# Performance work log

Measured on AMD Instinct MI355X. Metric: run time of the kernel, lower is better.

The kernel has to match this reference:

```python
import jax, jax.numpy as jnp
import numpy as np
import math

B, D, H, N, L = 32, 64, 8, 4096, 12
DK = D // H  # 8
APT = 10

def conv1x1_relu(x, w, b):
    # x: [B, C, N, L]; w: [O, C]; b: [O]  (1x1 conv == channel matmul)
    return jax.nn.relu(jnp.einsum('oc,bcnl->bonl', w, x) + b[None, :, None, None])

def setup_inputs() -> dict:
    key = jax.random.key(0)
    ks = jax.random.split(key, 12)
    s = 1.0 / math.sqrt(D)
    return {
        'x': jax.random.normal(ks[0], (B, D, N, L), jnp.float32),
        'wq': jax.random.normal(ks[1], (D, D), jnp.float32) * s,
        'bq': jnp.zeros((D,), jnp.float32),
        'wv': jax.random.normal(ks[2], (D, D), jnp.float32) * s,
        'bv': jnp.zeros((D,), jnp.float32),
        'wc': jax.random.normal(ks[3], (D, D), jnp.float32) * s,
        'bc': jnp.zeros((D,), jnp.float32),
        'memory': jax.random.normal(ks[4], (H, L, N, DK), jnp.float32) * 0.02,
        'weight': jnp.ones((D, N, L), jnp.float32),
        'bias': jnp.zeros((D, N, L), jnp.float32),
        'nv1': jax.random.normal(ks[5], (N, APT), jnp.float32),
        'nv2': jax.random.normal(ks[6], (APT, N), jnp.float32),
    }

def reference(x, wq, bq, wv, bv, wc, bc, memory, weight, bias, nv1, nv2):
    scale = 1.0 / math.sqrt(DK)
    q = conv1x1_relu(x, wq, bq)               # [B, D, N, L]
    v = conv1x1_relu(x, wv, bv)               # [B, D, N, L]
    # [B, D, N, L] -> [B, H, dk, N, L] -> [B, H, L, N, dk]
    v5 = jnp.transpose(v.reshape(B, H, DK, N, L), (0, 1, 4, 3, 2))
    q5 = jnp.transpose(q.reshape(B, H, DK, N, L), (0, 1, 4, 3, 2))
    key_sm = jax.nn.softmax(memory * scale, axis=-1)       # [H, L, N, dk]
    q_sm = jax.nn.softmax(q5 * scale, axis=-1)             # [B, H, L, N, dk]
    Aapt = jax.nn.softmax(jax.nn.relu(nv1 @ nv2), axis=-1) # [N, N]
    kv = jnp.einsum('hlnx,bhlny->bhlxy', key_sm, v5)       # [B,H,L,dk,dk]
    attn_qkv = jnp.einsum('bhlnx,bhlxy->bhlny', q_sm, kv)  # [B,H,L,N,dk]
    # 'nm,bhlnc->bhlnc' sums Aapt over m -> row-sum scaling of value
    row = jnp.sum(Aapt, axis=1)                            # [N]
    attn_dyn = row[None, None, None, :, None] * v5
    y = attn_qkv + attn_dyn                                # [B,H,L,N,dk]
    y = jnp.transpose(y, (0, 1, 4, 3, 2)).reshape(B, D, N, L)
    y = conv1x1_relu(y, wc, bc)
    out = y * weight[None] + bias[None] + y
    return out
```

## Files before the change

### kernel.cpp

```cpp
#include <hip/hip_runtime.h>
#include <math.h>
#include <stdint.h>

#define BB 32
#define DD 64
#define HH 8
#define NNN 4096
#define LL 12
#define PP (NNN * LL)

#define NTILES_A 24
#define CHUNK_A (64 * NTILES_A)
#define NCHUNK_A (PP / CHUNK_A)

#define NTILES_B 12
#define CHUNK_B (64 * NTILES_B)
#define NCHUNK_B (PP / CHUNK_B)

#define VSTRIDE 68
#define SCALE 0.35355339059327373f

typedef const __attribute__((address_space(1))) uint32_t gu32;
typedef __attribute__((address_space(3))) uint32_t lu32;

__device__ __forceinline__ void dma16(const float* src, float* dst) {
    __builtin_amdgcn_global_load_lds((gu32*)src, (lu32*)dst, 16, 0, 0);
}

__global__ void prep(const float* __restrict__ wq, const float* __restrict__ wv,
                     const float* __restrict__ wc, float* __restrict__ wt)
{
    const int i = blockIdx.x * 256 + threadIdx.x;
    const int o = i >> 6, c = i & 63;
    wt[c * 64 + o]        = wq[i];
    wt[4096 + c * 64 + o] = wv[i];
    wt[8192 + c * 64 + o] = wc[i];
}

__global__ void prep_ksm(const float* __restrict__ mem, float* __restrict__ ksm)
{
    const int g = blockIdx.x * 256 + threadIdx.x;
    const int p = g >> 3, h = g & 7;
    const int n = p / 12, l = p - n * 12;
    const float4* mp = (const float4*)(mem + (((size_t)(h * 12 + l) * NNN + n) << 3));
    float4 a0 = mp[0], a1 = mp[1];
    float v0 = a0.x * SCALE, v1 = a0.y * SCALE, v2 = a0.z * SCALE, v3 = a0.w * SCALE;
    float v4 = a1.x * SCALE, v5 = a1.y * SCALE, v6 = a1.z * SCALE, v7 = a1.w * SCALE;
    float m = fmaxf(fmaxf(fmaxf(v0, v1), fmaxf(v2, v3)),
                    fmaxf(fmaxf(v4, v5), fmaxf(v6, v7)));
    float e0 = __expf(v0 - m), e1 = __expf(v1 - m), e2 = __expf(v2 - m), e3 = __expf(v3 - m);
    float e4 = __expf(v4 - m), e5 = __expf(v5 - m), e6 = __expf(v6 - m), e7 = __expf(v7 - m);
    float inv = 1.0f / (e0 + e1 + e2 + e3 + e4 + e5 + e6 + e7);
    float4* op = (float4*)(ksm + ((size_t)g << 3));
    op[0] = make_float4(e0 * inv, e1 * inv, e2 * inv, e3 * inv);
    op[1] = make_float4(e4 * inv, e5 * inv, e6 * inv, e7 * inv);
}

__global__ void prep_wb(const float* __restrict__ wgt, const float* __restrict__ bsa,
                        float* __restrict__ wb)
{
    const size_t i = (size_t)blockIdx.x * 256 + threadIdx.x;
    wb[i * 2]     = wgt[i] + 1.0f;
    wb[i * 2 + 1] = bsa[i];
}

__global__ __launch_bounds__(512, 2)
void pass_a(const float* __restrict__ x, const float* __restrict__ wvt,
            const float* __restrict__ bv, const float* __restrict__ mem,
            const float* __restrict__ ksm,
            float* __restrict__ kv)
{
    __shared__ float xb0[64 * 64];
    __shared__ float xb1[64 * 64];
    __shared__ float ksl[64 * 64];
    __shared__ float v_tile[64 * VSTRIDE];

    const int t = threadIdx.x;
    const int b = blockIdx.y;
    const int chunk0 = blockIdx.x * CHUNK_A;

    const int p1 = t & 63;
    const int og = t >> 6;
    const int o0 = og << 3;
    const int o0u = __builtin_amdgcn_readfirstlane(o0);
    const float* __restrict__ wvu = wvt + o0u;

    float bvl[8];
#pragma unroll
    for (int j = 0; j < 8; j++) bvl[j] = bv[o0 + j];

    const int wid = t >> 6;
    const int ln  = t & 63;
    const int g_r = ln >> 4;
    const int g_c4 = (ln & 15) << 2;

    const int h2 = (t >> 3) & 7;
    const int x2 = t & 7;
    const int l0 = t >> 6;
    const int l1 = 8 + (t >> 6);
    const bool has2 = (t < 256);

    float acc[2][8];
#pragma unroll
    for (int q = 0; q < 2; q++)
#pragma unroll
        for (int y = 0; y < 8; y++) acc[q][y] = 0.f;

    const float* xb = x + (size_t)(b * 64) * PP;

    auto issue_x = [&](float* dst, int pn) {
        const int r0 = wid << 3;
        dma16(xb + (size_t)(r0 + g_r) * PP + pn + g_c4, dst + (r0 << 6));
        dma16(xb + (size_t)(r0 + 4 + g_r) * PP + pn + g_c4, dst + ((r0 + 4) << 6));
    };
    auto issue_ks = [&](int pn) {
        const int fo = wid << 9;
        const float* s0 = ksm + (((size_t)pn) << 6) + fo + (ln << 2);
        dma16(s0, ksl + fo);
        dma16(s0 + 256, ksl + fo + 256);
    };
    auto fallback_ks = [&](int pbase) {
        int pos = t >> 3, h = t & 7;
        int pg = pbase + pos;
        int n = pg / 12;
        int l = pg - n * 12;
        const float4* mp = (const float4*)(mem + (((size_t)(h * 12 + l) * NNN + n) << 3));
        float4 a0 = mp[0], a1 = mp[1];
        float v0 = a0.x * SCALE, v1 = a0.y * SCALE, v2 = a0.z * SCALE, v3 = a0.w * SCALE;
        float v4 = a1.x * SCALE, v5 = a1.y * SCALE, v6 = a1.z * SCALE, v7 = a1.w * SCALE;
        float m = fmaxf(fmaxf(fmaxf(v0, v1), fmaxf(v2, v3)),
                        fmaxf(fmaxf(v4, v5), fmaxf(v6, v7)));
        float e0 = __expf(v0 - m), e1 = __expf(v1 - m), e2 = __expf(v2 - m), e3 = __expf(v3 - m);
        float e4 = __expf(v4 - m), e5 = __expf(v5 - m), e6 = __expf(v6 - m), e7 = __expf(v7 - m);
        float inv = 1.0f / (e0 + e1 + e2 + e3 + e4 + e5 + e6 + e7);
        float4* kp = (float4*)(ksl + (pos << 6) + (h << 3));
        kp[0] = make_float4(e0 * inv, e1 * inv, e2 * inv, e3 * inv);
        kp[1] = make_float4(e4 * inv, e5 * inv, e6 * inv, e7 * inv);
    };

    issue_x(xb0, chunk0);
    if (ksm) issue_ks(chunk0); else fallback_ks(chunk0);
    __syncthreads();

    for (int tile = 0; tile < NTILES_A; tile++) {
        const int pbase = chunk0 + tile * 64;
        float* bufA = (tile & 1) ? xb1 : xb0;
        float* bufB = (tile & 1) ? xb0 : xb1;
        const bool more = (tile + 1) < NTILES_A;

        if (more) issue_x(bufB, pbase + 64);

        float va[8];
#pragma unroll
        for (int j = 0; j < 8; j++) va[j] = 0.f;
        for (int c = 0; c < 64; c += 4) {
            float xs0 = bufA[(c << 6) + p1];
            float xs1 = bufA[((c + 1) << 6) + p1];
            float xs2 = bufA[((c + 2) << 6) + p1];
            float xs3 = bufA[((c + 3) << 6) + p1];
            const float* w0 = wvu + c * 64;
#pragma unroll
            for (int j = 0; j < 8; j++) {
                va[j] += w0[j] * xs0;
                va[j] += w0[64 + j] * xs1;
                va[j] += w0[128 + j] * xs2;
                va[j] += w0[192 + j] * xs3;
            }
        }
        {
            const int slot = ((og ^ (p1 >> 3)) & 7) << 3;
            float4* vt4 = (float4*)(v_tile + p1 * VSTRIDE + slot);
            float4 w;
            w.x = fmaxf(va[0] + bvl[0], 0.f);
            w.y = fmaxf(va[1] + bvl[1], 0.f);
            w.z = fmaxf(va[2] + bvl[2], 0.f);
            w.w = fmaxf(va[3] + bvl[3], 0.f);
            vt4[0] = w;
            w.x = fmaxf(va[4] + bvl[4], 0.f);
            w.y = fmaxf(va[5] + bvl[5], 0.f);
            w.z = fmaxf(va[6] + bvl[6], 0.f);
            w.w = fmaxf(va[7] + bvl[7], 0.f);
            vt4[1] = w;
        }
        __syncthreads();

        const int r = pbase % 12;
        {
            int s = l0 - r;
            if (s < 0) s += 12;
            for (int p = s; p < 64; p += 12) {
                float ksv = ksl[(p << 6) + (h2 << 3) + x2];
                const int slot = ((h2 ^ (p >> 3)) & 7) << 3;
                const float4* vp = (const float4*)(v_tile + p * VSTRIDE + slot);
                float4 u0 = vp[0], u1 = vp[1];
                acc[0][0] += ksv * u0.x; acc[0][1] += ksv * u0.y;
                acc[0][2] += ksv * u0.z; acc[0][3] += ksv * u0.w;
                acc[0][4] += ksv * u1.x; acc[0][5] += ksv * u1.y;
                acc[0][6] += ksv * u1.z; acc[0][7] += ksv * u1.w;
            }
        }
        if (has2) {
            int s = l1 - r;
            if (s < 0) s += 12;
            for (int p = s; p < 64; p += 12) {
                float ksv = ksl[(p << 6) + (h2 << 3) + x2];
                const int slot = ((h2 ^ (p >> 3)) & 7) << 3;
                const float4* vp = (const float4*)(v_tile + p * VSTRIDE + slot);
                float4 u0 = vp[0], u1 = vp[1];
                acc[1][0] += ksv * u0.x; acc[1][1] += ksv * u0.y;
                acc[1][2] += ksv * u0.z; acc[1][3] += ksv * u0.w;
                acc[1][4] += ksv * u1.x; acc[1][5] += ksv * u1.y;
                acc[1][6] += ksv * u1.z; acc[1][7] += ksv * u1.w;
            }
        }
        __syncthreads();

        if (more) { if (ksm) issue_ks(pbase + 64); else fallback_ks(pbase + 64); }
    }

    {
        float* kvp = kv + (((size_t)((b * 12 + l0) * 8 + h2)) << 6) + (x2 << 3);
#pragma unroll
        for (int y = 0; y < 8; y++) atomicAdd(kvp + y, acc[0][y]);
    }
    if (has2) {
        float* kvp = kv + (((size_t)((b * 12 + l1) * 8 + h2)) << 6) + (x2 << 3);
#pragma unroll
        for (int y = 0; y < 8; y++) atomicAdd(kvp + y, acc[1][y]);
    }
}

__global__ __launch_bounds__(256, 4)
void pass_b(const float* __restrict__ x, const float* __restrict__ wqt,
            const float* __restrict__ wvt, const float* __restrict__ wct,
            const float* __restrict__ bq, const float* __restrict__ bv,
            const float* __restrict__ bc, const float* __restrict__ kv,
            const float* __restrict__ wgt, const float* __restrict__ bsa,
            const float* __restrict__ wb,
            float* __restrict__ out)
{
    __shared__ float kv_lds[12 * 512];
    __shared__ float y_tile[64 * 64];

    const int t = threadIdx.x;
    const int b = blockIdx.y;
    const int chunk0 = blockIdx.x * CHUNK_B;

    const int p1 = t & 63;
    const int og = t >> 6;
    const int o0 = og << 4;
    const int o0u = __builtin_amdgcn_readfirstlane(o0);
    const float* __restrict__ wqu = wqt + o0u;
    const float* __restrict__ wvu = wvt + o0u;
    const float* __restrict__ wcu = wct + o0u;

    {
        const float* kvb = kv + (size_t)b * 6144;
        for (int i = t; i < 6144; i += 256) {
            const int l = i >> 9;
            const int h = (i >> 6) & 7;
            const int xx = (i >> 3) & 7;
            const int y = i & 7;
            kv_lds[(l << 9) + (h << 6) + ((xx ^ (l & 3)) << 3) + y] = kvb[i];
        }
    }

    float bql[16], bvl[16], bcl[16];
#pragma unroll
    for (int j = 0; j < 16; j++) {
        bql[j] = bq[o0 + j];
        bvl[j] = bv[o0 + j];
        bcl[j] = bc[o0 + j];
    }

    const float* xb = x + (size_t)(b * 64) * PP;
    float* ob = out + (size_t)(b * 64) * PP;

    __syncthreads();

    for (int tile_i = 0; tile_i < NTILES_B; tile_i++) {
        const int pbase = chunk0 + tile_i * 64;
        const int pg = pbase + p1;
        const int l = pg % 12;

        float qa[16], va[16];
#pragma unroll
        for (int j = 0; j < 16; j++) { qa[j] = 0.f; va[j] = 0.f; }
        const float* xp = xb + pg;
        for (int c = 0; c < 64; c += 4) {
            float xs0 = xp[(size_t)c * PP];
            float xs1 = xp[(size_t)(c + 1) * PP];
            float xs2 = xp[(size_t)(c + 2) * PP];
            float xs3 = xp[(size_t)(c + 3) * PP];
            const float* q0 = wqu + c * 64;
            const float* v0 = wvu + c * 64;
#pragma unroll
            for (int j = 0; j < 16; j++) {
                qa[j] += q0[j] * xs0;       va[j] += v0[j] * xs0;
                qa[j] += q0[64 + j] * xs1;  va[j] += v0[64 + j] * xs1;
                qa[j] += q0[128 + j] * xs2; va[j] += v0[128 + j] * xs2;
                qa[j] += q0[192 + j] * xs3; va[j] += v0[192 + j] * xs3;
            }
        }
#pragma unroll
        for (int j = 0; j < 16; j++) {
            qa[j] = fmaxf(qa[j] + bql[j], 0.f) * SCALE;
            va[j] = fmaxf(va[j] + bvl[j], 0.f);
        }

#pragma unroll
        for (int hh = 0; hh < 2; hh++) {
            float* qh = qa + hh * 8;
            float m = fmaxf(fmaxf(fmaxf(qh[0], qh[1]), fmaxf(qh[2], qh[3])),
                            fmaxf(fmaxf(qh[4], qh[5]), fmaxf(qh[6], qh[7])));
            float s = 0.f;
#pragma unroll
            for (int xk = 0; xk < 8; xk++) { qh[xk] = __expf(qh[xk] - m); s += qh[xk]; }
            float inv = 1.0f / s;
#pragma unroll
            for (int xk = 0; xk < 8; xk++) qh[xk] *= inv;
        }

        const int lsw = l & 3;
#pragma unroll
        for (int hh = 0; hh < 2; hh++) {
            const int h = og * 2 + hh;
            const float* kvp = kv_lds + (l << 9) + (h << 6);
            float yv[8];
#pragma unroll
            for (int y = 0; y < 8; y++) yv[y] = va[hh * 8 + y];
#pragma unroll
            for (int xk = 0; xk < 8; xk++) {
                float qv = qa[hh * 8 + xk];
                const float4* kp = (const float4*)(kvp + ((xk ^ lsw) << 3));
                float4 k0 = kp[0], k1 = kp[1];
                yv[0] += qv * k0.x; yv[1] += qv * k0.y;
                yv[2] += qv * k0.z; yv[3] += qv * k0.w;
                yv[4] += qv * k1.x; yv[5] += qv * k1.y;
                yv[6] += qv * k1.z; yv[7] += qv * k1.w;
            }
#pragma unroll
            for (int y = 0; y < 8; y++)
                y_tile[((o0 + hh * 8 + y) << 6) + p1] = yv[y];
        }
        __syncthreads();

        float ca[16];
#pragma unroll
        for (int j = 0; j < 16; j++) ca[j] = 0.f;
        for (int c = 0; c < 64; c += 4) {
            float y0 = y_tile[(c << 6) + p1];
            float y1 = y_tile[((c + 1) << 6) + p1];
            float y2 = y_tile[((c + 2) << 6) + p1];
            float y3 = y_tile[((c + 3) << 6) + p1];
            const float* w0 = wcu + c * 64;
#pragma unroll
            for (int j = 0; j < 16; j++) {
                ca[j] += w0[j] * y0;
                ca[j] += w0[64 + j] * y1;
                ca[j] += w0[128 + j] * y2;
                ca[j] += w0[192 + j] * y3;
            }
        }
        if (wb) {
#pragma unroll
            for (int j = 0; j < 16; j++) {
                float yc = fmaxf(ca[j] + bcl[j], 0.f);
                size_t oi = (size_t)(o0 + j) * PP + pg;
                float2 w2 = *(const float2*)(wb + oi * 2);
                ob[oi] = yc * w2.x + w2.y;
            }
        } else {
#pragma unroll
            for (int j = 0; j < 16; j++) {
                float yc = fmaxf(ca[j] + bcl[j], 0.f);
                size_t oi = (size_t)(o0 + j) * PP + pg;
                ob[oi] = yc * (wgt[oi] + 1.0f) + bsa[oi];
            }
        }
        __syncthreads();
    }
}

extern "C" void kernel_launch(void* const* d_in, const int* in_sizes, int n_in,
                              void* d_out, int out_size, void* d_ws, size_t ws_size,
                              hipStream_t stream) {
    const float* x   = (const float*)d_in[0];
    const float* wq  = (const float*)d_in[1];
    const float* bq  = (const float*)d_in[2];
    const float* wv  = (const float*)d_in[3];
    const float* bv  = (const float*)d_in[4];
    const float* wc  = (const float*)d_in[5];
    const float* bc  = (const float*)d_in[6];
    const float* mem = (const float*)d_in[7];
    const float* wgt = (const float*)d_in[8];
    const float* bsa = (const float*)d_in[9];
    float* outp = (float*)d_out;

    const size_t kv_floats  = (size_t)BB * LL * HH * 64;
    const size_t wt_floats  = 3 * 4096;
    const size_t ksm_floats = (size_t)PP * 64;
    const size_t wb_floats  = (size_t)PP * 64 * 2;

    float* kvw = (float*)d_ws;
    float* wt  = kvw + kv_floats;
    float* ksm = wt + wt_floats;
    float* wb  = ksm + ksm_floats;
    const bool have_ksm =
        ws_size >= (kv_floats + wt_floats + ksm_floats) * sizeof(float);
    const bool have_wb =
        ws_size >= (kv_floats + wt_floats + ksm_floats + wb_floats) * sizeof(float);

    hipMemsetAsync(kvw, 0, kv_floats * sizeof(float), stream);

    prep<<<16, 256, 0, stream>>>(wq, wv, wc, wt);
    if (have_ksm) {
        prep_ksm<<<(PP * 8) / 256, 256, 0, stream>>>(mem, ksm);
    }
    if (have_wb) {
        prep_wb<<<(PP * 64) / 256, 256, 0, stream>>>(wgt, bsa, wb);
    }

    dim3 grid_a(NCHUNK_A, BB);
    pass_a<<<grid_a, 512, 0, stream>>>(x, wt + 4096, bv, mem,
                                       have_ksm ? ksm : nullptr, kvw);
    dim3 grid_b(NCHUNK_B, BB);
    pass_b<<<grid_b, 256, 0, stream>>>(x, wt, wt + 4096, wt + 8192,
                                       bq, bv, bc, kvw, wgt, bsa,
                                       have_wb ? wb : nullptr, outp);
}
```

Baseline: 1.584 ms.

## Stage x tiles in swizzled LDS with register prefetch of next tile in pass_b

pass_b now loads each 64x64 x tile cooperatively with float4 global loads into a transposed, XOR-swizzled LDS buffer. The next tile is prefetched into registers while the output conv runs, then written to LDS before the barrier. The y tile uses the same swizzled layout, so both channel loops read a float4 per four channels instead of four scalar LDS or global loads. Launch bounds drop to 2 blocks per SM to make room for the extra registers and LDS, at the cost of lower occupancy.

```diff
diff --git a/kernel.cpp b/kernel.cpp
--- a/kernel.cpp
+++ b/kernel.cpp
@@ -25,6 +25,10 @@
 
 __device__ __forceinline__ void dma16(const float* src, float* dst) {
     __builtin_amdgcn_global_load_lds((gu32*)src, (lu32*)dst, 16, 0, 0);
+}
+
+__device__ __forceinline__ int xsw(int p, int c4) {
+    return (p << 6) + (((c4 ^ (p & 7)) & 15) << 2);
 }
 
 __global__ void prep(const float* __restrict__ wq, const float* __restrict__ wv,
@@ -230,7 +234,7 @@
     }
 }
 
-__global__ __launch_bounds__(256, 4)
+__global__ __launch_bounds__(256, 2)
 void pass_b(const float* __restrict__ x, const float* __restrict__ wqt,
             const float* __restrict__ wvt, const float* __restrict__ wct,
             const float* __restrict__ bq, const float* __restrict__ bv,
@@ -239,8 +243,9 @@
             const float* __restrict__ wb,
             float* __restrict__ out)
 {
+    __shared__ float xt[64 * 64];
+    __shared__ float yt[64 * 64];
     __shared__ float kv_lds[12 * 512];
-    __shared__ float y_tile[64 * 64];
 
     const int t = threadIdx.x;
     const int b = blockIdx.y;
@@ -253,6 +258,20 @@
     const float* __restrict__ wqu = wqt + o0u;
     const float* __restrict__ wvu = wvt + o0u;
     const float* __restrict__ wcu = wct + o0u;
+
+    const int sx_c  = t >> 4;
+    const int sx_p4 = (t & 15) << 2;
+
+    float bql[16], bvl[16], bcl[16];
+#pragma unroll
+    for (int j = 0; j < 16; j++) {
+        bql[j] = bq[o0 + j];
+        bvl[j] = bv[o0 + j];
+        bcl[j] = bc[o0 + j];
+    }
+
+    const float* xb = x + (size_t)(b * 64) * PP;
+    float* ob = out + (size_t)(b * 64) * PP;
 
     {
         const float* kvb = kv + (size_t)b * 6144;
@@ -263,43 +282,37 @@
             const int y = i & 7;
             kv_lds[(l << 9) + (h << 6) + ((xx ^ (l & 3)) << 3) + y] = kvb[i];
         }
-    }
-
-    float bql[16], bvl[16], bcl[16];
-#pragma unroll
-    for (int j = 0; j < 16; j++) {
-        bql[j] = bq[o0 + j];
-        bvl[j] = bv[o0 + j];
-        bcl[j] = bc[o0 + j];
-    }
-
-    const float* xb = x + (size_t)(b * 64) * PP;
-    float* ob = out + (size_t)(b * 64) * PP;
-
+#pragma unroll
+        for (int r = 0; r < 4; r++) {
+            const int c = r * 16 + sx_c;
+            float4 a = *(const float4*)(xb + (size_t)c * PP + chunk0 + sx_p4);
+            xt[xsw(sx_p4 + 0, c >> 2) + (c & 3)] = a.x;
+            xt[xsw(sx_p4 + 1, c >> 2) + (c & 3)] = a.y;
+            xt[xsw(sx_p4 + 2, c >> 2) + (c & 3)] = a.z;
+            xt[xsw(sx_p4 + 3, c >> 2) + (c & 3)] = a.w;
+        }
+    }
     __syncthreads();
 
     for (int tile_i = 0; tile_i < NTILES_B; tile_i++) {
         const int pbase = chunk0 + tile_i * 64;
         const int pg = pbase + p1;
         const int l = pg % 12;
+        const bool more = (tile_i + 1) < NTILES_B;
 
         float qa[16], va[16];
 #pragma unroll
         for (int j = 0; j < 16; j++) { qa[j] = 0.f; va[j] = 0.f; }
-        const float* xp = xb + pg;
         for (int c = 0; c < 64; c += 4) {
-            float xs0 = xp[(size_t)c * PP];
-            float xs1 = xp[(size_t)(c + 1) * PP];
-            float xs2 = xp[(size_t)(c + 2) * PP];
-            float xs3 = xp[(size_t)(c + 3) * PP];
+            const float4 xv = *(const float4*)(xt + xsw(p1, c >> 2));
             const float* q0 = wqu + c * 64;
             const float* v0 = wvu + c * 64;
 #pragma unroll
             for (int j = 0; j < 16; j++) {
-                qa[j] += q0[j] * xs0;       va[j] += v0[j] * xs0;
-                qa[j] += q0[64 + j] * xs1;  va[j] += v0[64 + j] * xs1;
-                qa[j] += q0[128 + j] * xs2; va[j] += v0[128 + j] * xs2;
-                qa[j] += q0[192 + j] * xs3; va[j] += v0[192 + j] * xs3;
+                qa[j] += q0[j] * xv.x;       va[j] += v0[j] * xv.x;
+                qa[j] += q0[64 + j] * xv.y;  va[j] += v0[64 + j] * xv.y;
+                qa[j] += q0[128 + j] * xv.z; va[j] += v0[128 + j] * xv.z;
+                qa[j] += q0[192 + j] * xv.w; va[j] += v0[192 + j] * xv.w;
             }
         }
 #pragma unroll
@@ -322,44 +335,54 @@
         }
 
         const int lsw = l & 3;
+        float yv[2][8];
 #pragma unroll
         for (int hh = 0; hh < 2; hh++) {
             const int h = og * 2 + hh;
             const float* kvp = kv_lds + (l << 9) + (h << 6);
-            float yv[8];
-#pragma unroll
-            for (int y = 0; y < 8; y++) yv[y] = va[hh * 8 + y];
+#pragma unroll
+            for (int y = 0; y < 8; y++) yv[hh][y] = va[hh * 8 + y];
 #pragma unroll
             for (int xk = 0; xk < 8; xk++) {
                 float qv = qa[hh * 8 + xk];
                 const float4* kp = (const float4*)(kvp + ((xk ^ lsw) << 3));
                 float4 k0 = kp[0], k1 = kp[1];
-                yv[0] += qv * k0.x; yv[1] += qv * k0.y;
-                yv[2] += qv * k0.z; yv[3] += qv * k0.w;
-                yv[4] += qv * k1.x; yv[5] += qv * k1.y;
-                yv[6] += qv * k1.z; yv[7] += qv * k1.w;
-            }
-#pragma unroll
-            for (int y = 0; y < 8; y++)
-                y_tile[((o0 + hh * 8 + y) << 6) + p1] = yv[y];
+                yv[hh][0] += qv * k0.x; yv[hh][1] += qv * k0.y;
+                yv[hh][2] += qv * k0.z; yv[hh][3] += qv * k0.w;
+                yv[hh][4] += qv * k1.x; yv[hh][5] += qv * k1.y;
+                yv[hh][6] += qv * k1.z; yv[hh][7] += qv * k1.w;
+            }
+        }
+        {
+            const int oq = og << 2;
+            *(float4*)(yt + xsw(p1, oq + 0)) = make_float4(yv[0][0], yv[0][1], yv[0][2], yv[0][3]);
+            *(float4*)(yt + xsw(p1, oq + 1)) = make_float4(yv[0][4], yv[0][5], yv[0][6], yv[0][7]);
+            *(float4*)(yt + xsw(p1, oq + 2)) = make_float4(yv[1][0], yv[1][1], yv[1][2], yv[1][3]);
+            *(float4*)(yt + xsw(p1, oq + 3)) = make_float4(yv[1][4], yv[1][5], yv[1][6], yv[1][7]);
         }
         __syncthreads();
+
+        float4 st0, st1, st2, st3;
+        if (more) {
+            const int pn = pbase + 64;
+            st0 = *(const float4*)(xb + (size_t)(sx_c) * PP + pn + sx_p4);
+            st1 = *(const float4*)(xb + (size_t)(sx_c + 16) * PP + pn + sx_p4);
+            st2 = *(const float4*)(xb + (size_t)(sx_c + 32) * PP + pn + sx_p4);
+            st3 = *(const float4*)(xb + (size_t)(sx_c + 48) * PP + pn + sx_p4);
+        }
 
         float ca[16];
 #pragma unroll
         for (int j = 0; j < 16; j++) ca[j] = 0.f;
         for (int c = 0; c < 64; c += 4) {
-            float y0 = y_tile[(c << 6) + p1];
-            float y1 = y_tile[((c + 1) << 6) + p1];
-            float y2 = y_tile[((c + 2) << 6) + p1];
-            float y3 = y_tile[((c + 3) << 6) + p1];
+            const float4 yv4 = *(const float4*)(yt + xsw(p1, c >> 2));
             const float* w0 = wcu + c * 64;
 #pragma unroll
             for (int j = 0; j < 16; j++) {
-                ca[j] += w0[j] * y0;
-                ca[j] += w0[64 + j] * y1;
-                ca[j] += w0[128 + j] * y2;
-                ca[j] += w0[192 + j] * y3;
+                ca[j] += w0[j] * yv4.x;
+                ca[j] += w0[64 + j] * yv4.y;
+                ca[j] += w0[128 + j] * yv4.z;
+                ca[j] += w0[192 + j] * yv4.w;
             }
         }
         if (wb) {
@@ -377,6 +400,26 @@
                 size_t oi = (size_t)(o0 + j) * PP + pg;
                 ob[oi] = yc * (wgt[oi] + 1.0f) + bsa[oi];
             }
+        }
+
+        if (more) {
+            const int c0 = sx_c, c1 = sx_c + 16, c2 = sx_c + 32, c3 = sx_c + 48;
+            xt[xsw(sx_p4 + 0, c0 >> 2) + (c0 & 3)] = st0.x;
+            xt[xsw(sx_p4 + 1, c0 >> 2) + (c0 & 3)] = st0.y;
+            xt[xsw(sx_p4 + 2, c0 >> 2) + (c0 & 3)] = st0.z;
+            xt[xsw(sx_p4 + 3, c0 >> 2) + (c0 & 3)] = st0.w;
+            xt[xsw(sx_p4 + 0, c1 >> 2) + (c1 & 3)] = st1.x;
+            xt[xsw(sx_p4 + 1, c1 >> 2) + (c1 & 3)] = st1.y;
+            xt[xsw(sx_p4 + 2, c1 >> 2) + (c1 & 3)] = st1.z;
+            xt[xsw(sx_p4 + 3, c1 >> 2) + (c1 & 3)] = st1.w;
+            xt[xsw(sx_p4 + 0, c2 >> 2) + (c2 & 3)] = st2.x;
+            xt[xsw(sx_p4 + 1, c2 >> 2) + (c2 & 3)] = st2.y;
+            xt[xsw(sx_p4 + 2, c2 >> 2) + (c2 & 3)] = st2.z;
+            xt[xsw(sx_p4 + 3, c2 >> 2) + (c2 & 3)] = st2.w;
+            xt[xsw(sx_p4 + 0, c3 >> 2) + (c3 & 3)] = st3.x;
+            xt[xsw(sx_p4 + 1, c3 >> 2) + (c3 & 3)] = st3.y;
+            xt[xsw(sx_p4 + 2, c3 >> 2) + (c3 & 3)] = st3.z;
+            xt[xsw(sx_p4 + 3, c3 >> 2) + (c3 & 3)] = st3.w;
         }
         __syncthreads();
     }
```

After: 1.590 ms. No clear change (+0.4%).
